# Performance work log

Measured on AMD Instinct MI355X. Metric: run time of the kernel, lower is better.

## Reference

```python
import jax, jax.numpy as jnp
import numpy as np

D_MODEL, D_STATE, D_CONV, D_INNER = 1024, 16, 4, 2048
BATCH, SEQ = 4, 2048


def silu(v):
    return v * jax.nn.sigmoid(v)


def setup_inputs() -> dict:
    key = jax.random.key(0)
    ks = jax.random.split(key, 7)
    x = jax.random.normal(ks[0], (BATCH, SEQ, D_MODEL), dtype=jnp.float32)
    s = 0.02
    W_in = jax.random.normal(ks[1], (D_MODEL, 2 * D_INNER), dtype=jnp.float32) * s
    conv_w = jax.random.normal(ks[2], (D_INNER, 1, D_CONV), dtype=jnp.float32) * s  # depthwise (O, I/g=1, K)
    conv_b = jax.random.normal(ks[3], (D_INNER,), dtype=jnp.float32) * s
    W_xproj = jax.random.normal(ks[4], (D_INNER, 2 * D_STATE + 1), dtype=jnp.float32) * s
    A_log = jnp.log(jnp.tile(jnp.arange(1, D_STATE + 1, dtype=jnp.float32), (D_INNER, 1)))
    D = jnp.ones((D_INNER,), dtype=jnp.float32)
    W_out = jax.random.normal(ks[5], (D_INNER, D_MODEL), dtype=jnp.float32) * s
    return {"x": x, "W_in": W_in, "conv_w": conv_w, "conv_b": conv_b,
            "W_xproj": W_xproj, "A_log": A_log, "D": D, "W_out": W_out}


def reference(x, W_in, conv_w, conv_b, W_xproj, A_log, D, W_out):
    B, L, _ = x.shape
    xz = x @ W_in                                   # (B, L, 2*d_inner)
    x_proj, z = jnp.split(xz, 2, axis=-1)
    # Depthwise causal conv: padding=d_conv-1 then truncate to L == left-pad only.
    xc = jax.lax.conv_general_dilated(
        x_proj.transpose(0, 2, 1), conv_w,
        window_strides=(1,), padding=[(D_CONV - 1, 0)],
        feature_group_count=D_INNER,
        dimension_numbers=("NCH", "OIH", "NCH"))
    x_conv = silu((xc + conv_b[None, :, None]).transpose(0, 2, 1))  # (B, L, d_inner)
    ssm = x_conv @ W_xproj                           # (B, L, 1+2*d_state)
    delta = jax.nn.softplus(ssm[..., 0])             # (B, L)
    Bm = ssm[..., 1:1 + D_STATE]                     # (B, L, d_state)
    Cm = ssm[..., 1 + D_STATE:]                      # (B, L, d_state)
    # Original: deltaA = exp(delta*A) and softmax weights are computed but unused.
    deltaB = delta[..., None] * Bm                   # (B, L, d_state)
    # h_approx = mean_L(x outer deltaB): avoid (B,L,d_inner,d_state) intermediate.
    h_mean = jnp.einsum("bld,bln->bdn", x_conv, deltaB) / L  # (B, d_inner, d_state)
    y = jnp.einsum("bdn,bln->bld", h_mean, Cm)       # (B, L, d_inner)
    y = y + D[None, None, :] * x_conv
    y = y * silu(z)
    return y @ W_out                                 # (B, L, d_model)
```

## Files before the change

kernel.cpp:

```cpp
#include <hip/hip_runtime.h>
#include <hip/hip_bf16.h>
#include <stdint.h>

typedef __bf16 bf16x8 __attribute__((ext_vector_type(8)));
typedef float f32x4 __attribute__((ext_vector_type(4)));
typedef unsigned short u16;
typedef u16 ushort4v __attribute__((ext_vector_type(4)));
typedef u16 ushort8v __attribute__((ext_vector_type(8)));

__device__ __forceinline__ u16 f2bf(float f) {
    union { float f; uint32_t u; } v; v.f = f;
    uint32_t u = v.u + 0x7FFFu + ((v.u >> 16) & 1u);
    return (u16)(u >> 16);
}
__device__ __forceinline__ float bf2f(u16 b) {
    union { uint32_t u; float f; } v; v.u = ((uint32_t)b) << 16;
    return v.f;
}
__device__ __forceinline__ float silu_f(float v) {
    return v / (1.0f + __expf(-v));
}
__device__ __forceinline__ void gload_lds16(const u16* g, u16* l) {
    __builtin_amdgcn_global_load_lds(
        (const __attribute__((address_space(1))) void*)g,
        (__attribute__((address_space(3))) void*)l, 16, 0, 0);
}

__device__ __forceinline__ void trans_tile(
        const float* __restrict__ src, u16* __restrict__ dst, int R, int C,
        int bc, int br, float (*tt)[33], int tid) {
    const int tx = tid & 31, ty = tid >> 5;
#pragma unroll
    for (int i = 0; i < 4; i++)
        tt[ty + i * 8][tx] = src[(int64_t)(br * 32 + ty + i * 8) * C + bc * 32 + tx];
    __syncthreads();
#pragma unroll
    for (int i = 0; i < 4; i++)
        dst[(int64_t)(bc * 32 + ty + i * 8) * R + br * 32 + tx] = f2bf(tt[tx][ty + i * 8]);
}

__global__ __launch_bounds__(256) void prep_k(
        const float* __restrict__ x, u16* __restrict__ x_bf,
        const float* __restrict__ Wi, u16* __restrict__ Wti,
        const float* __restrict__ Wo, u16* __restrict__ Wto,
        const float* __restrict__ wx, u16* __restrict__ wxt) {
    __shared__ float tt[32][33];
    const int blk = blockIdx.x, tid = threadIdx.x;
    if (blk < 8192) {
        int i = blk * 256 + tid;
        float4 v = *(const float4*)&x[(int64_t)i * 4];
        ushort4v o = { f2bf(v.x), f2bf(v.y), f2bf(v.z), f2bf(v.w) };
        *(ushort4v*)&x_bf[(int64_t)i * 4] = o;
    } else if (blk < 12288) {
        int t = blk - 8192;
        trans_tile(Wi, Wti, 1024, 4096, t & 127, t >> 7, tt, tid);
    } else if (blk < 14336) {
        int t = blk - 12288;
        trans_tile(Wo, Wto, 2048, 1024, t & 31, t >> 5, tt, tid);
    } else {
        int idx = (blk - 14336) * 256 + tid;
        int j = idx >> 11, d = idx & 2047;
        wxt[idx] = (j < 33) ? f2bf(wx[d * 33 + j]) : (u16)0;
    }
}

template<int M_REP, int WARPS_M, int B_HALVES, bool OUT_BF16>
__global__ __launch_bounds__(512) void gemm_dp(
        const u16* __restrict__ A, const u16* __restrict__ Bt,
        void* __restrict__ Cout, int nbn_sh, int NT, int lda, int ldb, int ldc) {
    constexpr int WARPS_N = 8 / WARPS_M;
    constexpr int QPT = M_REP / 2;
    constexpr int WV_M = M_REP * 16;
    constexpr int BN = WARPS_N * 64;
    constexpr int B_T = BN * 64;

    __shared__ __align__(16) u16 As[2 * 16384];
    __shared__ __align__(16) u16 Bs[2 * B_T];

    const int tid = threadIdx.x;
    const int wave = tid >> 6;
    const int lane = tid & 63;
    const int wm = wave / WARPS_N, wn = wave % WARPS_N;
    const int fr = lane & 15, fq = lane >> 4;

    const int nwg = gridDim.x;
    const int cpx = nwg >> 3;
    const int swz = (blockIdx.x & 7) * cpx + (blockIdx.x >> 3);
    const int bm = swz >> nbn_sh;
    const int bn = swz & ((1 << nbn_sh) - 1);

    const int srow = tid >> 3;
    const int scol8 = ((tid & 7) ^ (srow & 7)) * 8;
    const u16* gA = A + (int64_t)(bm * 256 + srow) * lda + scol8;
    const u16* gB = Bt + (int64_t)(bn * BN + srow) * ldb + scol8;
    const int64_t lda64 = lda, ldb64 = ldb;

    const int ksw0 = ((fq) ^ (fr & 7)) * 8;
    const int ksw1 = ((4 + fq) ^ (fr & 7)) * 8;
    const int arow0 = (wm * WV_M + fr) * 64;
    const int brow0 = (wn * 64 + fr) * 64;

    auto STAGE_A_HALF = [&](int kt, int buf, int h) {
#pragma unroll
        for (int j = 0; j < 2; ++j)
            gload_lds16(gA + (int64_t)(h * 128 + j * 64) * lda64 + kt * 64,
                        &As[buf * 16384 + h * 8192 + j * 4096 + tid * 8]);
    };
    auto STAGE_B_HALF = [&](int kt, int buf, int h) {
#pragma unroll
        for (int j = 0; j < 2; ++j)
            gload_lds16(gB + (int64_t)(h * 128 + j * 64) * ldb64 + kt * 64,
                        &Bs[buf * B_T + h * 8192 + j * 4096 + tid * 8]);
    };

    f32x4 acc[M_REP][4] = {};

    STAGE_A_HALF(0, 0, 0); STAGE_A_HALF(0, 0, 1);
#pragma unroll
    for (int h = 0; h < B_HALVES; ++h) STAGE_B_HALF(0, 0, h);
#pragma unroll
    for (int h = 0; h < B_HALVES; ++h) STAGE_B_HALF(1, 1, h);
    if constexpr (B_HALVES == 2) { asm volatile("s_waitcnt vmcnt(4)" ::: "memory"); }
    else                         { asm volatile("s_waitcnt vmcnt(2)" ::: "memory"); }
    __builtin_amdgcn_s_barrier();

    const int NI = NT >> 1;
    for (int s = 0; s < NI; ++s) {
        const bool more = (s + 1 < NI);
#pragma unroll
        for (int t = 0; t < 2; ++t) {
            const u16* Ab = &As[t * 16384];
            const u16* Bb = &Bs[t * B_T];
            bf16x8 breg[4][2];
            bf16x8 areg[2][2][2];
#pragma unroll
            for (int q = 0; q < QPT; ++q) {
                const int p = q & 1;
                if (q == 0) {
#pragma unroll
                    for (int n = 0; n < 4; ++n) {
                        breg[n][0] = *(const bf16x8*)(Bb + brow0 + n * 1024 + ksw0);
                        breg[n][1] = *(const bf16x8*)(Bb + brow0 + n * 1024 + ksw1);
                    }
#pragma unroll
                    for (int j = 0; j < 2; ++j) {
                        areg[0][j][0] = *(const bf16x8*)(Ab + arow0 + j * 1024 + ksw0);
                        areg[0][j][1] = *(const bf16x8*)(Ab + arow0 + j * 1024 + ksw1);
                    }
                }
                __builtin_amdgcn_s_setprio(1);
                if (q + 1 < QPT) {
#pragma unroll
                    for (int j = 0; j < 2; ++j) {
                        areg[p ^ 1][j][0] = *(const bf16x8*)(Ab + arow0 + (2 * (q + 1) + j) * 1024 + ksw0);
                        areg[p ^ 1][j][1] = *(const bf16x8*)(Ab + arow0 + (2 * (q + 1) + j) * 1024 + ksw1);
                    }
                }
#pragma unroll
                for (int j = 0; j < 2; ++j)
#pragma unroll
                    for (int n = 0; n < 4; ++n) {
                        acc[2 * q + j][n] = __builtin_amdgcn_mfma_f32_16x16x32_bf16(
                            areg[p][j][0], breg[n][0], acc[2 * q + j][n], 0, 0, 0);
                        acc[2 * q + j][n] = __builtin_amdgcn_mfma_f32_16x16x32_bf16(
                            areg[p][j][1], breg[n][1], acc[2 * q + j][n], 0, 0, 0);
                    }
                if (q + 1 < QPT) {
#pragma unroll
                    for (int g = 0; g < 4; ++g) {
                        __builtin_amdgcn_sched_group_barrier(0x008, 2, 0);
                        __builtin_amdgcn_sched_group_barrier(0x100, 1, 0);
                        __builtin_amdgcn_sched_group_barrier(0x008, 2, 0);
                    }
                }
                __builtin_amdgcn_s_setprio(0);
                if constexpr (QPT == 4) {
                    if (t == 0 && q == 0)         STAGE_A_HALF(2 * s + 1, 1, 0);
                    if (t == 0 && q == 1)         STAGE_A_HALF(2 * s + 1, 1, 1);
                    if (t == 0 && q == 2 && more) STAGE_B_HALF(2 * s + 2, 0, 0);
                    if (t == 0 && q == 3 && more) STAGE_B_HALF(2 * s + 2, 0, 1);
                    if (t == 1 && q == 0 && more) STAGE_A_HALF(2 * s + 2, 0, 0);
                    if (t == 1 && q == 1 && more) STAGE_A_HALF(2 * s + 2, 0, 1);
                    if (t == 1 && q == 2 && more) STAGE_B_HALF(2 * s + 3, 1, 0);
                    if (t == 1 && q == 3 && more) STAGE_B_HALF(2 * s + 3, 1, 1);
                } else {
                    if (t == 0 && q == 0)         STAGE_A_HALF(2 * s + 1, 1, 0);
                    if (t == 0 && q == 1) {       STAGE_A_HALF(2 * s + 1, 1, 1);
                        if (more)                 STAGE_B_HALF(2 * s + 2, 0, 0); }
                    if (t == 1 && q == 0 && more) STAGE_A_HALF(2 * s + 2, 0, 0);
                    if (t == 1 && q == 1 && more) { STAGE_A_HALF(2 * s + 2, 0, 1);
                                                    STAGE_B_HALF(2 * s + 3, 1, 0); }
                }
                if (q == QPT - 1) {
                    if (more) {
                        if constexpr (B_HALVES == 2) { asm volatile("s_waitcnt vmcnt(4)" ::: "memory"); }
                        else                         { asm volatile("s_waitcnt vmcnt(2)" ::: "memory"); }
                    } else {
                        asm volatile("s_waitcnt vmcnt(0)" ::: "memory");
                    }
                }
                __builtin_amdgcn_s_barrier();
            }
        }
    }

#pragma unroll
    for (int m = 0; m < M_REP; ++m) {
#pragma unroll
        for (int n = 0; n < 4; ++n) {
            const int col = bn * BN + wn * 64 + n * 16 + fr;
#pragma unroll
            for (int r = 0; r < 4; ++r) {
                const int row = bm * 256 + wm * WV_M + m * 16 + fq * 4 + r;
                if constexpr (OUT_BF16)
                    ((u16*)Cout)[(int64_t)row * ldc + col] = f2bf(acc[m][n][r]);
                else
                    ((float*)Cout)[(int64_t)row * ldc + col] = acc[m][n][r];
            }
        }
    }
}

__global__ __launch_bounds__(256) void conv_silu_k(
        const u16* __restrict__ xz, const float* __restrict__ cw,
        const float* __restrict__ cb, u16* __restrict__ xc) {
    const int blk = blockIdx.x;
    const int b = blk >> 9;
    const int l0 = (blk & 511) << 2;
    const int d0 = threadIdx.x * 8;
    float w[8][4], bias[8];
#pragma unroll
    for (int j = 0; j < 8; j++) {
        float4 wv = *(const float4*)&cw[(d0 + j) * 4];
        w[j][0] = wv.x; w[j][1] = wv.y; w[j][2] = wv.z; w[j][3] = wv.w;
        bias[j] = cb[d0 + j];
    }
    float xp[7][8];
#pragma unroll
    for (int r = 0; r < 7; r++) {
        int l = l0 - 3 + r;
        if (l < 0) {
#pragma unroll
            for (int j = 0; j < 8; j++) xp[r][j] = 0.f;
        } else {
            ushort8v v = *(const ushort8v*)&xz[((int64_t)(b * 2048 + l)) * 4096 + d0];
#pragma unroll
            for (int j = 0; j < 8; j++) xp[r][j] = bf2f(v[j]);
        }
    }
#pragma unroll
    for (int li = 0; li < 4; li++) {
        ushort8v o;
#pragma unroll
        for (int j = 0; j < 8; j++) {
            float s = bias[j];
#pragma unroll
            for (int k = 0; k < 4; k++) s += w[j][k] * xp[li + k][j];
            o[j] = f2bf(silu_f(s));
        }
        *(ushort8v*)&xc[((int64_t)(b * 2048 + l0 + li)) * 2048 + d0] = o;
    }
}

__global__ __launch_bounds__(256) void ssm_proj_k(
        const u16* __restrict__ xc, const u16* __restrict__ wxt,
        float* __restrict__ spart) {
    const int gw = (blockIdx.x << 2) + (threadIdx.x >> 6);
    const int lane = threadIdx.x & 63;
    const int rb = gw >> 2, kc = gw & 3;
    const int fr = lane & 15, fq = lane >> 4;
    const u16* ap = xc + (int64_t)(rb * 16 + fr) * 2048 + kc * 512 + fq * 8;
    const u16* bp = wxt + (int64_t)fr * 2048 + kc * 512 + fq * 8;
    f32x4 acc0 = {}, acc1 = {}, acc2 = {};
#pragma unroll 4
    for (int k = 0; k < 512; k += 32) {
        bf16x8 av = *(const bf16x8*)(ap + k);
        bf16x8 b0 = *(const bf16x8*)(bp + k);
        bf16x8 b1 = *(const bf16x8*)(bp + 16 * 2048 + k);
        bf16x8 b2 = *(const bf16x8*)(bp + 32 * 2048 + k);
        acc0 = __builtin_amdgcn_mfma_f32_16x16x32_bf16(av, b0, acc0, 0, 0, 0);
        acc1 = __builtin_amdgcn_mfma_f32_16x16x32_bf16(av, b1, acc1, 0, 0, 0);
        acc2 = __builtin_amdgcn_mfma_f32_16x16x32_bf16(av, b2, acc2, 0, 0, 0);
    }
    float* sp = spart + ((int64_t)kc * 8192 + rb * 16) * 48;
#pragma unroll
    for (int r = 0; r < 4; r++) {
        int ro = (fq * 4 + r) * 48;
        sp[ro + fr] = acc0[r];
        sp[ro + 16 + fr] = acc1[r];
        sp[ro + 32 + fr] = acc2[r];
    }
}

__global__ __launch_bounds__(256) void ssm_fin_k(
        const float* __restrict__ spart, float* __restrict__ dB,
        float* __restrict__ Cm) {
    const int row = blockIdx.x * 256 + threadIdx.x;
    const float* sp = spart + (int64_t)row * 48;
    float s[33];
#pragma unroll
    for (int j = 0; j < 33; j++)
        s[j] = sp[j] + sp[8192 * 48 + j] + sp[2 * 8192 * 48 + j] + sp[3 * 8192 * 48 + j];
    float d0v = s[0];
    float delta = (d0v > 20.f) ? d0v : log1pf(__expf(d0v));
#pragma unroll
    for (int n = 0; n < 16; n++) {
        dB[(int64_t)row * 16 + n] = delta * s[1 + n] * (1.0f / 2048.0f);
        Cm[(int64_t)row * 16 + n] = s[17 + n];
    }
}

__global__ __launch_bounds__(256) void h_part_k(
        const u16* __restrict__ xc, const float* __restrict__ dB,
        float* __restrict__ hp) {
    const int blk = blockIdx.x;
    const int dt = blk & 7, b = (blk >> 3) & 3, lc = blk >> 5;
    const int d = dt * 256 + threadIdx.x;
    const u16* xp = xc + ((int64_t)(b * 2048 + lc * 256)) * 2048 + d;
    const float* dbp = dB + (int64_t)(b * 2048 + lc * 256) * 16;
    float acc[16] = {};
    for (int l = 0; l < 256; l++) {
        float xv = bf2f(xp[(int64_t)l * 2048]);
#pragma unroll
        for (int n = 0; n < 16; n++) acc[n] += xv * dbp[l * 16 + n];
    }
    float* o = hp + ((int64_t)((lc * 4 + b) * 2048 + d)) * 16;
#pragma unroll
    for (int n = 0; n < 16; n++) o[n] = acc[n];
}

__global__ void h_red_k(const float* __restrict__ hp, float* __restrict__ h) {
    const int i = blockIdx.x * 256 + threadIdx.x;
    float s = 0.f;
#pragma unroll
    for (int c = 0; c < 8; c++) s += hp[(int64_t)c * 131072 + i];
    h[i] = s;
}

__global__ __launch_bounds__(256) void y_gate_k(
        u16* __restrict__ xz, const u16* __restrict__ xc,
        const float* __restrict__ h, const float* __restrict__ Cm,
        const float* __restrict__ Dp) {
    const int blk = blockIdx.x;
    const int lc = blk & 63, dt = (blk >> 6) & 1, b = blk >> 7;
    const int d0 = dt * 1024 + threadIdx.x * 4;
    const float* hpp = h + ((int64_t)(b * 2048 + d0)) * 16;
    float hreg[4][16];
#pragma unroll
    for (int i = 0; i < 4; i++)
#pragma unroll
        for (int n = 0; n < 16; n++) hreg[i][n] = hpp[i * 16 + n];
    float Dv[4];
#pragma unroll
    for (int i = 0; i < 4; i++) Dv[i] = Dp[d0 + i];
    __shared__ float Cs[32][16];
    if (threadIdx.x < 128)
        ((float4*)&Cs[0][0])[threadIdx.x] =
            ((const float4*)(Cm + (int64_t)(b * 2048 + lc * 32) * 16))[threadIdx.x];
    __syncthreads();
    for (int li = 0; li < 32; li++) {
        const int64_t rowz = (int64_t)(b * 2048 + lc * 32 + li);
        ushort4v xcv = *(const ushort4v*)&xc[rowz * 2048 + d0];
        ushort4v zv = *(const ushort4v*)&xz[rowz * 4096 + 2048 + d0];
        ushort4v o;
#pragma unroll
        for (int i = 0; i < 4; i++) {
            float s = Dv[i] * bf2f(xcv[i]);
#pragma unroll
            for (int n = 0; n < 16; n++) s += hreg[i][n] * Cs[li][n];
            o[i] = f2bf(s * silu_f(bf2f(zv[i])));
        }
        *(ushort4v*)&xz[rowz * 4096 + d0] = o;
    }
}

extern "C" void kernel_launch(void* const* d_in, const int* in_sizes, int n_in,
                              void* d_out, int out_size, void* d_ws, size_t ws_size,
                              hipStream_t stream) {
    (void)in_sizes; (void)n_in; (void)out_size; (void)ws_size;
    const float* x      = (const float*)d_in[0];
    const float* W_in   = (const float*)d_in[1];
    const float* conv_w = (const float*)d_in[2];
    const float* conv_b = (const float*)d_in[3];
    const float* W_xp   = (const float*)d_in[4];
    const float* Dp     = (const float*)d_in[6];
    const float* W_out  = (const float*)d_in[7];
    float* out = (float*)d_out;
    char* ws = (char*)d_ws;

    u16*   x_bf   = (u16*)(ws);
    float* spart  = (float*)(ws);
    float* dB     = (float*)(ws + 6291456);
    float* Cm     = (float*)(ws + 6815744);
    float* hp     = (float*)(ws + 7340032);
    float* h      = (float*)(ws + 11534336);
    u16*   Wt_in  = (u16*)(ws + 16777216);
    u16*   Wt_out = (u16*)(ws + 25165824);
    u16*   Wxt    = (u16*)(ws + 29360128);
    u16*   xz     = (u16*)(ws + 29556736);
    u16*   xcv    = (u16*)(ws + 96665600);

    prep_k<<<14720, 256, 0, stream>>>(x, x_bf, W_in, Wt_in, W_out, Wt_out, W_xp, Wxt);
    gemm_dp<8, 2, 2, true><<<512, 512, 0, stream>>>(x_bf, Wt_in, xz, 4, 16, 1024, 1024, 4096);
    conv_silu_k<<<2048, 256, 0, stream>>>(xz, conv_w, conv_b, xcv);
    ssm_proj_k<<<512, 256, 0, stream>>>(xcv, Wxt, spart);
    ssm_fin_k<<<32, 256, 0, stream>>>(spart, dB, Cm);
    h_part_k<<<256, 256, 0, stream>>>(xcv, dB, hp);
    h_red_k<<<512, 256, 0, stream>>>(hp, h);
    y_gate_k<<<512, 256, 0, stream>>>(xz, xcv, h, Cm, Dp);
    gemm_dp<4, 4, 1, false><<<256, 512, 0, stream>>>(xz, Wt_out, out, 3, 32, 4096, 2048, 1024);
}
```

Before: 241.6 us.

## Fuse conv+SiLU with SSM projection and finalize; split h partials finer

Merges the depthwise conv/SiLU, the x_proj MFMA GEMM and the delta/B/C finalize into one kernel. Each block computes 16 rows of conv output, stages them in LDS and multiplies against W_xproj from there, then reduces the four K-chunk partials in shared memory. This removes two launches, the partial-sum buffer round trip through global memory, and the reread of xc. It also splits h_part into four times as many L-chunks for more parallelism, with a correspondingly longer reduction in h_red. The cost is a large LDS footprint per block, which limits occupancy.

```diff
diff --git a/kernel.cpp b/kernel.cpp
--- a/kernel.cpp
+++ b/kernel.cpp
@@ -4,6 +4,7 @@
 
 typedef __bf16 bf16x8 __attribute__((ext_vector_type(8)));
 typedef float f32x4 __attribute__((ext_vector_type(4)));
+typedef float f32x2 __attribute__((ext_vector_type(2)));
 typedef unsigned short u16;
 typedef u16 ushort4v __attribute__((ext_vector_type(4)));
 typedef u16 ushort8v __attribute__((ext_vector_type(8)));
@@ -221,13 +222,20 @@
     }
 }
 
-__global__ __launch_bounds__(256) void conv_silu_k(
+__global__ __launch_bounds__(256) void conv_ssm_k(
         const u16* __restrict__ xz, const float* __restrict__ cw,
-        const float* __restrict__ cb, u16* __restrict__ xc) {
+        const float* __restrict__ cb, const u16* __restrict__ wxt,
+        u16* __restrict__ xc, float* __restrict__ dB, float* __restrict__ Cm) {
+    __shared__ __align__(16) u16 Xs[16][2064];
+    __shared__ float Sred[4][16][48];
+    __shared__ float deltas[16];
     const int blk = blockIdx.x;
-    const int b = blk >> 9;
-    const int l0 = (blk & 511) << 2;
-    const int d0 = threadIdx.x * 8;
+    const int b = blk >> 7, lb = blk & 127;
+    const int l0 = lb << 4;
+    const int64_t r0 = (int64_t)b * 2048 + l0;
+    const int tid = threadIdx.x;
+    const int d0 = tid * 8;
+
     float w[8][4], bias[8];
 #pragma unroll
     for (int j = 0; j < 8; j++) {
@@ -235,42 +243,42 @@
         w[j][0] = wv.x; w[j][1] = wv.y; w[j][2] = wv.z; w[j][3] = wv.w;
         bias[j] = cb[d0 + j];
     }
-    float xp[7][8];
-#pragma unroll
-    for (int r = 0; r < 7; r++) {
+    float win[4][8];
+#pragma unroll
+    for (int r = 0; r < 3; r++) {
         int l = l0 - 3 + r;
         if (l < 0) {
 #pragma unroll
-            for (int j = 0; j < 8; j++) xp[r][j] = 0.f;
+            for (int j = 0; j < 8; j++) win[r][j] = 0.f;
         } else {
-            ushort8v v = *(const ushort8v*)&xz[((int64_t)(b * 2048 + l)) * 4096 + d0];
-#pragma unroll
-            for (int j = 0; j < 8; j++) xp[r][j] = bf2f(v[j]);
+            ushort8v v = *(const ushort8v*)&xz[((int64_t)b * 2048 + l) * 4096 + d0];
+#pragma unroll
+            for (int j = 0; j < 8; j++) win[r][j] = bf2f(v[j]);
         }
     }
 #pragma unroll
-    for (int li = 0; li < 4; li++) {
+    for (int li = 0; li < 16; li++) {
+        ushort8v v = *(const ushort8v*)&xz[(r0 + li) * 4096 + d0];
+#pragma unroll
+        for (int j = 0; j < 8; j++) win[(3 + li) & 3][j] = bf2f(v[j]);
         ushort8v o;
 #pragma unroll
         for (int j = 0; j < 8; j++) {
             float s = bias[j];
 #pragma unroll
-            for (int k = 0; k < 4; k++) s += w[j][k] * xp[li + k][j];
+            for (int k = 0; k < 4; k++) s += w[j][k] * win[(li + k) & 3][j];
             o[j] = f2bf(silu_f(s));
         }
-        *(ushort8v*)&xc[((int64_t)(b * 2048 + l0 + li)) * 2048 + d0] = o;
-    }
-}
-
-__global__ __launch_bounds__(256) void ssm_proj_k(
-        const u16* __restrict__ xc, const u16* __restrict__ wxt,
-        float* __restrict__ spart) {
-    const int gw = (blockIdx.x << 2) + (threadIdx.x >> 6);
-    const int lane = threadIdx.x & 63;
-    const int rb = gw >> 2, kc = gw & 3;
+        *(ushort8v*)&xc[(r0 + li) * 2048 + d0] = o;
+        *(ushort8v*)&Xs[li][d0] = o;
+    }
+    __syncthreads();
+
+    const int kc = tid >> 6;
+    const int lane = tid & 63;
     const int fr = lane & 15, fq = lane >> 4;
-    const u16* ap = xc + (int64_t)(rb * 16 + fr) * 2048 + kc * 512 + fq * 8;
     const u16* bp = wxt + (int64_t)fr * 2048 + kc * 512 + fq * 8;
+    const u16* ap = &Xs[fr][kc * 512 + fq * 8];
     f32x4 acc0 = {}, acc1 = {}, acc2 = {};
 #pragma unroll 4
     for (int k = 0; k < 512; k += 32) {
@@ -282,31 +290,26 @@
         acc1 = __builtin_amdgcn_mfma_f32_16x16x32_bf16(av, b1, acc1, 0, 0, 0);
         acc2 = __builtin_amdgcn_mfma_f32_16x16x32_bf16(av, b2, acc2, 0, 0, 0);
     }
-    float* sp = spart + ((int64_t)kc * 8192 + rb * 16) * 48;
 #pragma unroll
     for (int r = 0; r < 4; r++) {
-        int ro = (fq * 4 + r) * 48;
-        sp[ro + fr] = acc0[r];
-        sp[ro + 16 + fr] = acc1[r];
-        sp[ro + 32 + fr] = acc2[r];
-    }
-}
-
-__global__ __launch_bounds__(256) void ssm_fin_k(
-        const float* __restrict__ spart, float* __restrict__ dB,
-        float* __restrict__ Cm) {
-    const int row = blockIdx.x * 256 + threadIdx.x;
-    const float* sp = spart + (int64_t)row * 48;
-    float s[33];
-#pragma unroll
-    for (int j = 0; j < 33; j++)
-        s[j] = sp[j] + sp[8192 * 48 + j] + sp[2 * 8192 * 48 + j] + sp[3 * 8192 * 48 + j];
-    float d0v = s[0];
-    float delta = (d0v > 20.f) ? d0v : log1pf(__expf(d0v));
-#pragma unroll
-    for (int n = 0; n < 16; n++) {
-        dB[(int64_t)row * 16 + n] = delta * s[1 + n] * (1.0f / 2048.0f);
-        Cm[(int64_t)row * 16 + n] = s[17 + n];
+        Sred[kc][fq * 4 + r][fr]      = acc0[r];
+        Sred[kc][fq * 4 + r][16 + fr] = acc1[r];
+        Sred[kc][fq * 4 + r][32 + fr] = acc2[r];
+    }
+    __syncthreads();
+    if (tid < 16) {
+        float s0 = Sred[0][tid][0] + Sred[1][tid][0] + Sred[2][tid][0] + Sred[3][tid][0];
+        deltas[tid] = (s0 > 20.f) ? s0 : log1pf(__expf(s0));
+    }
+    __syncthreads();
+    {
+        const int row = tid >> 4, n = tid & 15;
+        float sB = Sred[0][row][1 + n] + Sred[1][row][1 + n] +
+                   Sred[2][row][1 + n] + Sred[3][row][1 + n];
+        float sC = Sred[0][row][17 + n] + Sred[1][row][17 + n] +
+                   Sred[2][row][17 + n] + Sred[3][row][17 + n];
+        dB[(r0 + row) * 16 + n] = deltas[row] * sB * (1.0f / 2048.0f);
+        Cm[(r0 + row) * 16 + n] = sC;
     }
 }
 
@@ -316,24 +319,24 @@
     const int blk = blockIdx.x;
     const int dt = blk & 7, b = (blk >> 3) & 3, lc = blk >> 5;
     const int d = dt * 256 + threadIdx.x;
-    const u16* xp = xc + ((int64_t)(b * 2048 + lc * 256)) * 2048 + d;
-    const float* dbp = dB + (int64_t)(b * 2048 + lc * 256) * 16;
-    float acc[16] = {};
-    for (int l = 0; l < 256; l++) {
+    const u16* xp = xc + ((int64_t)(b * 2048 + lc * 64)) * 2048 + d;
+    const f32x2* dbp = (const f32x2*)(dB + (int64_t)(b * 2048 + lc * 64) * 16);
+    f32x2 acc[8] = {};
+    for (int l = 0; l < 64; l++) {
         float xv = bf2f(xp[(int64_t)l * 2048]);
 #pragma unroll
-        for (int n = 0; n < 16; n++) acc[n] += xv * dbp[l * 16 + n];
+        for (int q = 0; q < 8; q++) acc[q] += dbp[l * 8 + q] * xv;
     }
     float* o = hp + ((int64_t)((lc * 4 + b) * 2048 + d)) * 16;
 #pragma unroll
-    for (int n = 0; n < 16; n++) o[n] = acc[n];
+    for (int q = 0; q < 8; q++) *(f32x2*)&o[q * 2] = acc[q];
 }
 
 __global__ void h_red_k(const float* __restrict__ hp, float* __restrict__ h) {
     const int i = blockIdx.x * 256 + threadIdx.x;
     float s = 0.f;
 #pragma unroll
-    for (int c = 0; c < 8; c++) s += hp[(int64_t)c * 131072 + i];
+    for (int c = 0; c < 32; c++) s += hp[(int64_t)c * 131072 + i];
     h[i] = s;
 }
 
@@ -389,11 +392,10 @@
     char* ws = (char*)d_ws;
 
     u16*   x_bf   = (u16*)(ws);
-    float* spart  = (float*)(ws);
-    float* dB     = (float*)(ws + 6291456);
-    float* Cm     = (float*)(ws + 6815744);
-    float* hp     = (float*)(ws + 7340032);
-    float* h      = (float*)(ws + 11534336);
+    float* dB     = (float*)(ws);
+    float* Cm     = (float*)(ws + 524288);
+    float* h      = (float*)(ws + 1048576);
+    float* hp     = (float*)(ws + 1572864);
     u16*   Wt_in  = (u16*)(ws + 16777216);
     u16*   Wt_out = (u16*)(ws + 25165824);
     u16*   Wxt    = (u16*)(ws + 29360128);
@@ -402,10 +404,8 @@
 
     prep_k<<<14720, 256, 0, stream>>>(x, x_bf, W_in, Wt_in, W_out, Wt_out, W_xp, Wxt);
     gemm_dp<8, 2, 2, true><<<512, 512, 0, stream>>>(x_bf, Wt_in, xz, 4, 16, 1024, 1024, 4096);
-    conv_silu_k<<<2048, 256, 0, stream>>>(xz, conv_w, conv_b, xcv);
-    ssm_proj_k<<<512, 256, 0, stream>>>(xcv, Wxt, spart);
-    ssm_fin_k<<<32, 256, 0, stream>>>(spart, dB, Cm);
-    h_part_k<<<256, 256, 0, stream>>>(xcv, dB, hp);
+    conv_ssm_k<<<512, 256, 0, stream>>>(xz, conv_w, conv_b, Wxt, xcv, dB, Cm);
+    h_part_k<<<1024, 256, 0, stream>>>(xcv, dB, hp);
     h_red_k<<<512, 256, 0, stream>>>(hp, h);
     y_gate_k<<<512, 256, 0, stream>>>(xz, xcv, h, Cm, Dp);
     gemm_dp<4, 4, 1, false><<<256, 512, 0, stream>>>(xz, Wt_out, out, 3, 32, 4096, 2048, 1024);
```

After: 209.8 us. 1.15x faster.
